# Performance work log

Hardware: AMD Instinct MI355X
Metric: run time of the kernel (lower is better)

The kernel has to match this reference:

```python
import jax, jax.numpy as jnp
import numpy as np

B, T, C = 2, 2048, 2048
NH, NKV, D = 16, 4, 128
N_REP = NH // NKV
THETA = 10000.0


def setup_inputs() -> dict:
    key = jax.random.key(0)
    ks = jax.random.split(key, 5)
    s = 0.02
    return {
        "x": jax.random.normal(ks[0], (B, T, C), dtype=jnp.float32),
        "Wq": jax.random.normal(ks[1], (C, C), dtype=jnp.float32) * s,
        "Wk": jax.random.normal(ks[2], (NKV * D, C), dtype=jnp.float32) * s,
        "Wv": jax.random.normal(ks[3], (NKV * D, C), dtype=jnp.float32) * s,
        "Wo": jax.random.normal(ks[4], (C, C), dtype=jnp.float32) * s,
    }


def _rope(t):
    # t: (B, H, T, D); rotate pairs (even, odd) by angle pos * theta_i
    inv_freq = 1.0 / (THETA ** (jnp.arange(0, D, 2, dtype=jnp.float32) / D))  # (D/2,)
    ang = jnp.arange(T, dtype=jnp.float32)[:, None] * inv_freq[None, :]       # (T, D/2)
    cos, sin = jnp.cos(ang), jnp.sin(ang)
    te, to = t[..., 0::2], t[..., 1::2]
    re = te * cos - to * sin
    ro = te * sin + to * cos
    return jnp.stack([re, ro], axis=-1).reshape(t.shape).astype(t.dtype)


def reference(x, Wq, Wk, Wv, Wo):
    # Projections (Linear: y = x @ W.T)
    q = (x @ Wq.T).reshape(B, T, NH, D).transpose(0, 2, 1, 3)    # (B,NH,T,D)
    k = (x @ Wk.T).reshape(B, T, NKV, D).transpose(0, 2, 1, 3)   # (B,NKV,T,D)
    v = (x @ Wv.T).reshape(B, T, NKV, D).transpose(0, 2, 1, 3)
    q = _rope(q)
    k = _rope(k)
    # GQA: group query heads per kv head instead of materializing repeated K/V
    qg = q.reshape(B, NKV, N_REP, T, D)                          # (B,G,R,T,D)
    scale = 1.0 / jnp.sqrt(jnp.float32(D))
    scores = jnp.einsum("bgrtd,bgsd->bgrts", qg, k) * scale      # (B,G,R,T,T)
    causal = jnp.tril(jnp.ones((T, T), dtype=bool))
    scores = jnp.where(causal, scores, jnp.finfo(scores.dtype).min)
    attn = jax.nn.softmax(scores, axis=-1)
    out = jnp.einsum("bgrts,bgsd->bgrtd", attn, v)               # (B,G,R,T,D)
    out = out.reshape(B, NH, T, D).transpose(0, 2, 1, 3).reshape(B, T, C)
    return out @ Wo.T
```

## Files before the change

### kernel.cpp

```cpp
#include <hip/hip_runtime.h>
#include <hip/hip_bf16.h>
#include <stdint.h>

#define B_   2
#define T_   2048
#define C_   2048
#define NH_  16
#define NKV_ 4
#define D_   128
#define NREP_ 4

typedef __attribute__((ext_vector_type(8))) short bf16x8;
typedef __attribute__((ext_vector_type(4))) float f32x4;

__device__ inline short f2bs(float f) {
    __hip_bfloat16 h = __float2bfloat16(f);
    return *reinterpret_cast<short*>(&h);
}

__device__ inline void gl_lds16(const __hip_bfloat16* g, __hip_bfloat16* l) {
    __builtin_amdgcn_global_load_lds(
        (const __attribute__((address_space(1))) unsigned int*)g,
        (__attribute__((address_space(3))) unsigned int*)l,
        16, 0, 0);
}

__global__ void prep_kernel(const float* __restrict__ x,  const float* __restrict__ Wq,
                            const float* __restrict__ Wk, const float* __restrict__ Wv,
                            const float* __restrict__ Wo,
                            __hip_bfloat16* __restrict__ xb, __hip_bfloat16* __restrict__ wcat,
                            __hip_bfloat16* __restrict__ wob, float2* __restrict__ ropeTab) {
    int tid = blockIdx.x * blockDim.x + threadIdx.x;
    const int CVT_THREADS = 4718592;
    if (tid < CVT_THREADS) {
        int i4 = tid * 4;
        const float* src;
        __hip_bfloat16* dst;
        int off;
        if (i4 < 8388608)       { src = x;  dst = xb;             off = i4; }
        else if (i4 < 12582912) { src = Wq; dst = wcat;           off = i4 - 8388608; }
        else if (i4 < 13631488) { src = Wk; dst = wcat + 4194304; off = i4 - 12582912; }
        else if (i4 < 14680064) { src = Wv; dst = wcat + 5242880; off = i4 - 13631488; }
        else                    { src = Wo; dst = wob;            off = i4 - 14680064; }
        float4 v = *reinterpret_cast<const float4*>(src + off);
        short4 o;
        o.x = f2bs(v.x); o.y = f2bs(v.y); o.z = f2bs(v.z); o.w = f2bs(v.w);
        *reinterpret_cast<short4*>(dst + off) = o;
    } else {
        int e = tid - CVT_THREADS;
        if (e < 131072) {
            int t = e >> 6, p = e & 63;
            float inv = __expf(-(float)p * (9.210340371976184f / 64.0f));
            float ang = (float)t * inv;
            ropeTab[e] = make_float2(cosf(ang), sinf(ang));
        }
    }
}

template <int MODE, int NTN>
__global__ __launch_bounds__(512, 2) void gemm256(
    const __hip_bfloat16* __restrict__ A,
    const __hip_bfloat16* __restrict__ Bm,
    const float2* __restrict__ ropeTab,
    __hip_bfloat16* __restrict__ qo,
    __hip_bfloat16* __restrict__ ko,
    __hip_bfloat16* __restrict__ vT,
    float* __restrict__ Cout) {
    constexpr int K = 2048;
    constexpr int NT = K / 64;
    extern __shared__ char lds[];

    const int tid = threadIdx.x;
    const int lane = tid & 63;
    const int wid = tid >> 6;
    const int wm = wid >> 2, wn = wid & 3;
    const int q16 = lane >> 4, r16 = lane & 15;

    const int cpx = (int)gridDim.x >> 3;
    const int bs = ((int)blockIdx.x & 7) * cpx + ((int)blockIdx.x >> 3);
    const int tm = bs / NTN, tn = bs % NTN;
    const int rmA = tm * 256, rmB = tn * 256;

    char* const aBuf0 = lds + wm * 16384;
    char* const aBuf1 = lds + 32768 + wm * 16384;
    char* const bBuf0 = lds + 65536 + (wn >> 1) * 16384;
    char* const bBuf1 = lds + 65536 + 32768 + (wn >> 1) * 16384;

    const int sw  = (r16 & 7) << 4;
    const int cS0 = (q16 << 4) ^ sw;
    const int cS1 = (64 | (q16 << 4)) ^ sw;
    const int rA128 = r16 * 128;
    const int rB128 = ((wn & 1) * 64 + r16) * 128;

    f32x4 acc[8][4] = {};
    bf16x8 aF[4][2], bF[2][2][2];

#define STG(Mp, rowbase, kstep, ldsoff)                                              \
    { _Pragma("unroll") for (int li = 0; li < 2; li++) {                             \
        const int L_ = li * 8192 + tid * 16;                                         \
        const int rw_ = L_ >> 7;                                                     \
        const int cb_ = (L_ & 127) ^ ((rw_ & 7) << 4);                               \
        gl_lds16(Mp + (size_t)((rowbase) + rw_) * K + (kstep) * 64 + (cb_ >> 1),     \
                 (__hip_bfloat16*)(lds + (ldsoff) + L_));                            \
    } }
#define RDA(base, a)                                                                 \
    { _Pragma("unroll") for (int mi = 0; mi < 4; mi++) {                             \
        const char* p_ = (base) + (a) * 8192 + mi * 2048 + rA128;                    \
        aF[mi][0] = *(const bf16x8*)(p_ + cS0);                                      \
        aF[mi][1] = *(const bf16x8*)(p_ + cS1);                                      \
    } }
#define RDB(base, b)                                                                 \
    { _Pragma("unroll") for (int nj = 0; nj < 2; nj++) {                             \
        const char* p_ = (base) + (b) * 4096 + nj * 2048 + rB128;                    \
        bF[b][nj][0] = *(const bf16x8*)(p_ + cS0);                                   \
        bF[b][nj][1] = *(const bf16x8*)(p_ + cS1);                                   \
    } }
#define MM(a, b)                                                                     \
    { _Pragma("unroll") for (int mi = 0; mi < 4; mi++)                               \
      _Pragma("unroll") for (int nj = 0; nj < 2; nj++) {                             \
        acc[(a)*4+mi][(b)*2+nj] = __builtin_amdgcn_mfma_f32_16x16x32_bf16(           \
            aF[mi][0], bF[(b)][nj][0], acc[(a)*4+mi][(b)*2+nj], 0, 0, 0);            \
        acc[(a)*4+mi][(b)*2+nj] = __builtin_amdgcn_mfma_f32_16x16x32_bf16(           \
            aF[mi][1], bF[(b)][nj][1], acc[(a)*4+mi][(b)*2+nj], 0, 0, 0);            \
    } }
#define BAR  __builtin_amdgcn_s_barrier()
#define LGK0 asm volatile("s_waitcnt lgkmcnt(0)" ::: "memory")
#define VM6  asm volatile("s_waitcnt vmcnt(6)" ::: "memory")
#define VM0  asm volatile("s_waitcnt vmcnt(0)" ::: "memory")
#define PRIO_MM(a, b)                                                                \
    __builtin_amdgcn_s_setprio(1); MM(a, b); __builtin_amdgcn_s_setprio(0)
#define STEP(AB_, BB_, S0_, S2_, S3a_, S3b_, VMW_)                                   \
    RDA(AB_, 0); RDB(BB_, 0); S0_;                                                   \
    BAR; LGK0; PRIO_MM(0, 0); BAR;                                                   \
    RDB(BB_, 1);                                                                     \
    BAR; LGK0; PRIO_MM(0, 1); BAR;                                                   \
    RDA(AB_, 1); S2_;                                                                \
    BAR; LGK0; PRIO_MM(1, 0); BAR;                                                   \
    S3a_; S3b_;                                                                      \
    BAR; LGK0; PRIO_MM(1, 1); VMW_; BAR;

    STG(A,  rmA,       0, 0);
    STG(A,  rmA + 128, 0, 16384);
    STG(Bm, rmB,       0, 65536);
    STG(Bm, rmB + 128, 0, 65536 + 16384);
    STG(A,  rmA,       1, 32768);
    STG(Bm, rmB,       1, 65536 + 32768);
    STG(Bm, rmB + 128, 1, 65536 + 32768 + 16384);
    VM6; BAR;

    for (int u = 0; u < NT - 2; u += 2) {
        STEP(aBuf0, bBuf0,
             STG(A,  rmA + 128, u + 1, 32768 + 16384),
             STG(Bm, rmB,       u + 2, 65536),
             STG(A,  rmA,       u + 2, 0),
             STG(Bm, rmB + 128, u + 2, 65536 + 16384),
             VM6)
        STEP(aBuf1, bBuf1,
             STG(A,  rmA + 128, u + 2, 16384),
             STG(Bm, rmB,       u + 3, 65536 + 32768),
             STG(A,  rmA,       u + 3, 32768),
             STG(Bm, rmB + 128, u + 3, 65536 + 32768 + 16384),
             VM6)
    }
    STEP(aBuf0, bBuf0,
         STG(A, rmA + 128, NT - 1, 32768 + 16384),
         ((void)0), ((void)0), ((void)0),
         VM0)
    STEP(aBuf1, bBuf1, ((void)0), ((void)0), ((void)0), ((void)0), ((void)0))

#undef STEP
#undef PRIO_MM
#undef VM0
#undef VM6
#undef LGK0
#undef BAR
#undef MM
#undef RDB
#undef RDA
#undef STG

    if constexpr (MODE == 0) {
        constexpr int N = NTN * 256;
        float* const cbase = Cout + (size_t)(rmA + wm * 128) * N + tn * 256 + wn * 64 + r16;
#pragma unroll
        for (int Ai = 0; Ai < 8; Ai++)
#pragma unroll
            for (int r = 0; r < 4; r++) {
                float* dst = cbase + (size_t)(Ai * 16 + q16 * 4 + r) * N;
#pragma unroll
                for (int Bi = 0; Bi < 4; Bi++)
                    dst[Bi * 16] = acc[Ai][Bi][r];
            }
    } else {
        const int hb = tn * 2 + (wn >> 1);
        const float sgn = (r16 & 1) ? 1.0f : -1.0f;
#pragma unroll
        for (int Ai = 0; Ai < 8; Ai++)
#pragma unroll
            for (int r = 0; r < 4; r++) {
                const int m = rmA + wm * 128 + Ai * 16 + q16 * 4 + r;
                const int bb = m >> 11, t = m & 2047;
                if (hb < 20) {
                    const float2* tabRow = ropeTab + t * 64;
                    __hip_bfloat16* dst = (hb < 16)
                        ? qo + ((size_t)(bb * NH_ + hb) * T_ + t) * D_
                        : ko + ((size_t)(bb * NKV_ + (hb - 16)) * T_ + t) * D_;
#pragma unroll
                    for (int Bi = 0; Bi < 4; Bi++) {
                        const int dloc = (wn & 1) * 64 + Bi * 16 + r16;
                        float v = acc[Ai][Bi][r];
                        float prt = __shfl_xor(v, 1);
                        float2 cs = tabRow[dloc >> 1];
                        dst[dloc] = __float2bfloat16(fmaf(prt * sgn, cs.y, v * cs.x));
                    }
                } else {
                    __hip_bfloat16* dst = vT + (size_t)(bb * NKV_ + (hb - 20)) * D_ * T_ + t;
#pragma unroll
                    for (int Bi = 0; Bi < 4; Bi++) {
                        const int dloc = (wn & 1) * 64 + Bi * 16 + r16;
                        dst[(size_t)dloc * T_] = __float2bfloat16(acc[Ai][Bi][r]);
                    }
                }
            }
    }
}

__global__ __launch_bounds__(256, 3) void attn_kernel(const __hip_bfloat16* __restrict__ Q,
                                                      const __hip_bfloat16* __restrict__ Kt,
                                                      const __hip_bfloat16* __restrict__ Vt,
                                                      __hip_bfloat16* __restrict__ Ao,
                                                      float* __restrict__ O0,
                                                      float* __restrict__ O1,
                                                      float* __restrict__ l0p,
                                                      float* __restrict__ l1p) {
    __shared__ __hip_bfloat16 Ks[2][4096];
    __shared__ __hip_bfloat16 Vs[2][4096];
    __shared__ __hip_bfloat16 Pl[4][1280];

    const int lane = threadIdx.x & 63, wv = threadIdx.x >> 6;
    const int bg = blockIdx.y;
    const int u  = (int)blockIdx.x;
    int tb, nIt, sIdx;
    if (u < 32)      { tb = u;      nIt = tb + 1;      sIdx = -1; }
    else if (u < 64) { tb = u;      nIt = 32;          sIdx = 0;  }
    else             { tb = u - 32; nIt = tb + 1 - 32; sIdx = 1;  }
    const int sBase = (sIdx == 1) ? 1024 : 0;
    const int b = bg >> 2, g = bg & 3;
    const int h = g * 4 + wv;
    const int t0 = tb * 32;
    const int q16 = lane >> 4, r16 = lane & 15;

    const __hip_bfloat16* qh = Q + ((size_t)((b * NH_ + h) * T_) + t0) * D_;
    const __hip_bfloat16* kh = Kt + (size_t)(b * NKV_ + g) * T_ * D_;
    const __hip_bfloat16* vh = Vt + (size_t)(b * NKV_ + g) * D_ * T_;

    bf16x8 bqA[4], bqB[4];
#pragma unroll
    for (int kk = 0; kk < 4; kk++) {
        bqA[kk] = *reinterpret_cast<const bf16x8*>(qh + (size_t)r16 * D_ + kk * 32 + q16 * 8);
        bqB[kk] = *reinterpret_cast<const bf16x8*>(qh + (size_t)(16 + r16) * D_ + kk * 32 + q16 * 8);
    }

    float liA = 0.f, liB = 0.f;
    f32x4 oA[8], oB[8];
#pragma unroll
    for (int d = 0; d < 8; d++) {
        oA[d] = (f32x4){0.f, 0.f, 0.f, 0.f};
        oB[d] = (f32x4){0.f, 0.f, 0.f, 0.f};
    }

    const float SCL2 = 0.088388347648318447f * 1.4426950408889634f;
    const int tqA = t0 + r16;
    const int tqB = t0 + 16 + r16;

    const __hip_bfloat16* gK = kh + (size_t)((wv & 1) * 16 + r16) * D_ + q16 * 8;
    const __hip_bfloat16* gV = vh + (size_t)(((wv - 2) * 4) * 16 + r16) * T_ + q16 * 8;

#define STAGE(bufi, s0_)                                                        \
    do {                                                                        \
        if (wv < 2) {                                                           \
            const __hip_bfloat16* gp = gK + (size_t)(s0_) * D_;                 \
            __hip_bfloat16* lp = &Ks[bufi][(wv * 4) * 512] + lane * 8;          \
            gl_lds16(gp,      lp);                                              \
            gl_lds16(gp + 32, lp + 512);                                        \
            gl_lds16(gp + 64, lp + 1024);                                      \
            gl_lds16(gp + 96, lp + 1536);                                      \
        } else {                                                                \
            const __hip_bfloat16* gp = gV + (s0_);                              \
            __hip_bfloat16* lp = &Vs[bufi][((wv - 2) * 4) * 512] + lane * 8;    \
            gl_lds16(gp,                      lp);                              \
            gl_lds16(gp + (size_t)16 * T_,    lp + 512);                        \
            gl_lds16(gp + (size_t)32 * T_,    lp + 1024);                      \
            gl_lds16(gp + (size_t)48 * T_,    lp + 1536);                      \
        }                                                                       \
    } while (0)

    STAGE(0, sBase);

    for (int j = 0; j < nIt; j++) {
        const int s0 = sBase + j * 32;
        const int cur = j & 1;
        __syncthreads();
        if (j + 1 < nIt) STAGE(cur ^ 1, s0 + 32);

        f32x4 sc0A = (f32x4){0.f, 0.f, 0.f, 0.f};
        f32x4 sc1A = (f32x4){0.f, 0.f, 0.f, 0.f};
        f32x4 sc0B = (f32x4){0.f, 0.f, 0.f, 0.f};
        f32x4 sc1B = (f32x4){0.f, 0.f, 0.f, 0.f};
        {
            bf16x8 ak[4];
#pragma unroll
            for (int kk = 0; kk < 4; kk++)
                ak[kk] = *reinterpret_cast<const bf16x8*>(&Ks[cur][kk * 512] + lane * 8);
#pragma unroll
            for (int kk = 0; kk < 4; kk++) {
                sc0A = __builtin_amdgcn_mfma_f32_16x16x32_bf16(ak[kk], bqA[kk], sc0A, 0, 0, 0);
                sc0B = __builtin_amdgcn_mfma_f32_16x16x32_bf16(ak[kk], bqB[kk], sc0B, 0, 0, 0);
            }
#pragma unroll
            for (int kk = 0; kk < 4; kk++)
                ak[kk] = *reinterpret_cast<const bf16x8*>(&Ks[cur][(4 + kk) * 512] + lane * 8);
#pragma unroll
            for (int kk = 0; kk < 4; kk++) {
                sc1A = __builtin_amdgcn_mfma_f32_16x16x32_bf16(ak[kk], bqA[kk], sc1A, 0, 0, 0);
                sc1B = __builtin_amdgcn_mfma_f32_16x16x32_bf16(ak[kk], bqB[kk], sc1B, 0, 0, 0);
            }
        }

        ushort4 w0A, w1A, w0B, w1B;
        float psA = 0.f, psB = 0.f;
        if (s0 + 32 > t0) {
#pragma unroll
            for (int r = 0; r < 4; r++) {
                int s_a = s0 + q16 * 4 + r;
                float pa0 = (s_a <= tqA)      ? __builtin_amdgcn_exp2f(sc0A[r] * SCL2) : 0.f;
                float pa1 = (s_a + 16 <= tqA) ? __builtin_amdgcn_exp2f(sc1A[r] * SCL2) : 0.f;
                float pb0 = (s_a <= tqB)      ? __builtin_amdgcn_exp2f(sc0B[r] * SCL2) : 0.f;
                float pb1 = (s_a + 16 <= tqB) ? __builtin_amdgcn_exp2f(sc1B[r] * SCL2) : 0.f;
                psA += pa0 + pa1;
                psB += pb0 + pb1;
                ((unsigned short*)&w0A)[r] = (unsigned short)f2bs(pa0);
                ((unsigned short*)&w1A)[r] = (unsigned short)f2bs(pa1);
                ((unsigned short*)&w0B)[r] = (unsigned short)f2bs(pb0);
                ((unsigned short*)&w1B)[r] = (unsigned short)f2bs(pb1);
            }
        } else {
#pragma unroll
            for (int r = 0; r < 4; r++) {
                float pa0 = __builtin_amdgcn_exp2f(sc0A[r] * SCL2);
                float pa1 = __builtin_amdgcn_exp2f(sc1A[r] * SCL2);
                float pb0 = __builtin_amdgcn_exp2f(sc0B[r] * SCL2);
                float pb1 = __builtin_amdgcn_exp2f(sc1B[r] * SCL2);
                psA += pa0 + pa1;
                psB += pb0 + pb1;
                ((unsigned short*)&w0A)[r] = (unsigned short)f2bs(pa0);
                ((unsigned short*)&w1A)[r] = (unsigned short)f2bs(pa1);
                ((unsigned short*)&w0B)[r] = (unsigned short)f2bs(pb0);
                ((unsigned short*)&w1B)[r] = (unsigned short)f2bs(pb1);
            }
        }
        liA += psA;
        liB += psB;

        *reinterpret_cast<ushort4*>(&Pl[wv][r16 * 40 + q16 * 4]) = w0A;
        *reinterpret_cast<ushort4*>(&Pl[wv][r16 * 40 + 16 + q16 * 4]) = w1A;
        *reinterpret_cast<ushort4*>(&Pl[wv][640 + r16 * 40 + q16 * 4]) = w0B;
        *reinterpret_cast<ushort4*>(&Pl[wv][640 + r16 * 40 + 16 + q16 * 4]) = w1B;
        asm volatile("s_waitcnt lgkmcnt(0)" ::: "memory");
        bf16x8 pfA = *reinterpret_cast<const bf16x8*>(&Pl[wv][r16 * 40 + q16 * 8]);
        bf16x8 pfB = *reinterpret_cast<const bf16x8*>(&Pl[wv][640 + r16 * 40 + q16 * 8]);

#pragma unroll
        for (int d = 0; d < 8; d++) {
            bf16x8 bv = *reinterpret_cast<const bf16x8*>(&Vs[cur][d * 512] + lane * 8);
            oA[d] = __builtin_amdgcn_mfma_f32_16x16x32_bf16(pfA, bv, oA[d], 0, 0, 0);
            oB[d] = __builtin_amdgcn_mfma_f32_16x16x32_bf16(pfB, bv, oB[d], 0, 0, 0);
        }
    }

    liA += __shfl_xor(liA, 16);
    liA += __shfl_xor(liA, 32);
    liB += __shfl_xor(liB, 16);
    liB += __shfl_xor(liB, 32);

    if (sIdx < 0) {
#pragma unroll
        for (int r = 0; r < 4; r++) {
            float lrA = __shfl(liA, q16 * 4 + r, 16);
            float lrB = __shfl(liB, q16 * 4 + r, 16);
            float invA = 1.0f / lrA;
            float invB = 1.0f / lrB;
            int tA = t0 + q16 * 4 + r;
            __hip_bfloat16* dstA = Ao + (size_t)(b * T_ + tA) * C_ + h * D_ + r16;
            __hip_bfloat16* dstB = dstA + (size_t)16 * C_;
#pragma unroll
            for (int d = 0; d < 8; d++) {
                dstA[d * 16] = __float2bfloat16(oA[d][r] * invA);
                dstB[d * 16] = __float2bfloat16(oB[d][r] * invB);
            }
        }
    } else {
        float* Os = (sIdx == 0) ? O0 : O1;
        float* ls = (sIdx == 0) ? l0p : l1p;
        const size_t rb = (size_t)(b * NH_ + h) * 1024 + (size_t)(t0 - 1024);
        if (q16 == 0) {
            ls[rb + r16]      = liA;
            ls[rb + 16 + r16] = liB;
        }
#pragma unroll
        for (int r = 0; r < 4; r++) {
            int rowl = q16 * 4 + r;
            float* dA = Os + (rb + rowl) * 128 + r16;
            float* dB = Os + (rb + 16 + rowl) * 128 + r16;
#pragma unroll
            for (int d = 0; d < 8; d++) {
                dA[d * 16] = oA[d][r];
                dB[d * 16] = oB[d][r];
            }
        }
    }
#undef STAGE
}

__global__ void attn_combine(const float* __restrict__ O0, const float* __restrict__ O1,
                             const float* __restrict__ l0, const float* __restrict__ l1,
                             __hip_bfloat16* __restrict__ Ao) {
    int idx = blockIdx.x * blockDim.x + threadIdx.x;
    int row = idx >> 5, d4 = (idx & 31) << 2;
    int bh = row >> 10, tl = row & 1023;
    int b = bh >> 4, h = bh & 15;
    float inv = 1.0f / (l0[row] + l1[row]);
    float4 a = *reinterpret_cast<const float4*>(O0 + (size_t)row * 128 + d4);
    float4 c = *reinterpret_cast<const float4*>(O1 + (size_t)row * 128 + d4);
    short4 o;
    o.x = f2bs((a.x + c.x) * inv);
    o.y = f2bs((a.y + c.y) * inv);
    o.z = f2bs((a.z + c.z) * inv);
    o.w = f2bs((a.w + c.w) * inv);
    *reinterpret_cast<short4*>(Ao + (size_t)(b * T_ + 1024 + tl) * C_ + h * D_ + d4) = o;
}

extern "C" void kernel_launch(void* const* d_in, const int* in_sizes, int n_in,
                              void* d_out, int out_size, void* d_ws, size_t ws_size,
                              hipStream_t stream) {
    const float* x  = (const float*)d_in[0];
    const float* Wq = (const float*)d_in[1];
    const float* Wk = (const float*)d_in[2];
    const float* Wv = (const float*)d_in[3];
    const float* Wo = (const float*)d_in[4];
    float* out = (float*)d_out;
    char* ws = (char*)d_ws;

    __hip_bfloat16* xb   = (__hip_bfloat16*)(ws + 0);
    __hip_bfloat16* wcat = (__hip_bfloat16*)(ws + 16777216);
    float2*         ropeTab = (float2*)(ws + 29360128);
    __hip_bfloat16* wob  = (__hip_bfloat16*)(ws + 30408704);
    __hip_bfloat16* qatt = (__hip_bfloat16*)(ws + 38797312);
    __hip_bfloat16* katt = (__hip_bfloat16*)(ws + 55574528);
    __hip_bfloat16* vT   = (__hip_bfloat16*)(ws + 59768832);
    __hip_bfloat16* aout = (__hip_bfloat16*)(ws + 63963136);
    float* O0 = (float*)(ws + 0);
    float* O1 = (float*)(ws + 80740352);
    float* l0 = (float*)(ws + 97517568);
    float* l1 = (float*)(ws + 97648640);

    static bool s_attr_done = false;
    if (!s_attr_done) {
        hipFuncSetAttribute(reinterpret_cast<const void*>(&gemm256<1, 12>),
                            hipFuncAttributeMaxDynamicSharedMemorySize, 131072);
        hipFuncSetAttribute(reinterpret_cast<const void*>(&gemm256<0, 8>),
                            hipFuncAttributeMaxDynamicSharedMemorySize, 131072);
        s_attr_done = true;
    }

    const int thr = 256;
    prep_kernel<<<18944, thr, 0, stream>>>(x, Wq, Wk, Wv, Wo, xb, wcat, wob, ropeTab);

    gemm256<1, 12><<<192, 512, 131072, stream>>>(xb, wcat, ropeTab, qatt, katt, vT, nullptr);

    attn_kernel<<<dim3(96, 8), 256, 0, stream>>>(qatt, katt, vT, aout, O0, O1, l0, l1);
    attn_combine<<<(2 * NH_ * 1024 * 32) / thr, thr, 0, stream>>>(O0, O1, l0, l1, aout);

    gemm256<0, 8><<<128, 512, 131072, stream>>>(aout, wob, nullptr, nullptr, nullptr, nullptr, out);
}
```

Measured before the change: 306.5 us.

## Rewrite GEMM pipeline with 32-wide k-slices and parametric N tile

Replaces the hand-scheduled four-phase GEMM mainloop with a simpler double-buffered loop that splits each 64-wide k-step into two 32-column slices, with a 4-row XOR swizzle, and issues the next step's loads before each MFMA batch. The kernel is templated on the N tile width so the output projection uses 256x128 tiles over 256 blocks with less LDS, instead of 128 blocks of 256x256. The aim is to fill more CUs for the small output GEMM and to simplify the overlap of loads and compute. In exchange it loses the fine-grained setprio and barrier interleaving, and the larger number of tiles increases operand reloads.

```diff
diff --git a/kernel.cpp b/kernel.cpp
--- a/kernel.cpp
+++ b/kernel.cpp
@@ -57,8 +57,8 @@
     }
 }
 
-template <int MODE, int NTN>
-__global__ __launch_bounds__(512, 2) void gemm256(
+template <int MODE, int BN, int NTN>
+__global__ __launch_bounds__(512, 2) void gemm_ff(
     const __hip_bfloat16* __restrict__ A,
     const __hip_bfloat16* __restrict__ Bm,
     const float2* __restrict__ ropeTab,
@@ -68,137 +68,117 @@
     float* __restrict__ Cout) {
     constexpr int K = 2048;
     constexpr int NT = K / 64;
+    constexpr int WN = BN / 64;
+    constexpr int WM = 8 / WN;
+    constexpr int RPW = 256 / WM;
+    constexpr int MI_T = RPW / 16;
+    constexpr int BSZ = BN * 64;
+    constexpr int BLOADS = BSZ / 8192;
     extern __shared__ char lds[];
 
     const int tid = threadIdx.x;
     const int lane = tid & 63;
     const int wid = tid >> 6;
-    const int wm = wid >> 2, wn = wid & 3;
+    const int wm = wid / WN, wn = wid % WN;
     const int q16 = lane >> 4, r16 = lane & 15;
 
     const int cpx = (int)gridDim.x >> 3;
     const int bs = ((int)blockIdx.x & 7) * cpx + ((int)blockIdx.x >> 3);
     const int tm = bs / NTN, tn = bs % NTN;
-    const int rmA = tm * 256, rmB = tn * 256;
-
-    char* const aBuf0 = lds + wm * 16384;
-    char* const aBuf1 = lds + 32768 + wm * 16384;
-    char* const bBuf0 = lds + 65536 + (wn >> 1) * 16384;
-    char* const bBuf1 = lds + 65536 + 32768 + (wn >> 1) * 16384;
-
-    const int sw  = (r16 & 7) << 4;
-    const int cS0 = (q16 << 4) ^ sw;
-    const int cS1 = (64 | (q16 << 4)) ^ sw;
-    const int rA128 = r16 * 128;
-    const int rB128 = ((wn & 1) * 64 + r16) * 128;
-
-    f32x4 acc[8][4] = {};
-    bf16x8 aF[4][2], bF[2][2][2];
-
-#define STG(Mp, rowbase, kstep, ldsoff)                                              \
+    const int rmA = tm * 256, rmB = tn * BN;
+
+    const int csw = (q16 << 4) ^ ((r16 & 3) << 4);
+
+    f32x4 acc[MI_T][4] = {};
+    bf16x8 aF[MI_T], bF[4];
+
+#define STG_A(buf_, sl_, kstep_)                                                     \
     { _Pragma("unroll") for (int li = 0; li < 2; li++) {                             \
         const int L_ = li * 8192 + tid * 16;                                         \
-        const int rw_ = L_ >> 7;                                                     \
-        const int cb_ = (L_ & 127) ^ ((rw_ & 7) << 4);                               \
-        gl_lds16(Mp + (size_t)((rowbase) + rw_) * K + (kstep) * 64 + (cb_ >> 1),     \
-                 (__hip_bfloat16*)(lds + (ldsoff) + L_));                            \
+        const int rw_ = L_ >> 6;                                                     \
+        const int cb_ = (L_ & 63) ^ ((rw_ & 3) << 4);                                \
+        gl_lds16(A + (size_t)(rmA + rw_) * K + (kstep_) * 64 + (sl_) * 32 + (cb_ >> 1), \
+                 (__hip_bfloat16*)(lds + (buf_) * 32768 + (sl_) * 16384 + L_));      \
     } }
-#define RDA(base, a)                                                                 \
-    { _Pragma("unroll") for (int mi = 0; mi < 4; mi++) {                             \
-        const char* p_ = (base) + (a) * 8192 + mi * 2048 + rA128;                    \
-        aF[mi][0] = *(const bf16x8*)(p_ + cS0);                                      \
-        aF[mi][1] = *(const bf16x8*)(p_ + cS1);                                      \
+#define STG_B(buf_, sl_, kstep_)                                                     \
+    { _Pragma("unroll") for (int li = 0; li < BLOADS; li++) {                        \
+        const int L_ = li * 8192 + tid * 16;                                         \
+        const int rw_ = L_ >> 6;                                                     \
+        const int cb_ = (L_ & 63) ^ ((rw_ & 3) << 4);                                \
+        gl_lds16(Bm + (size_t)(rmB + rw_) * K + (kstep_) * 64 + (sl_) * 32 + (cb_ >> 1), \
+                 (__hip_bfloat16*)(lds + 65536 + (buf_) * 2 * BSZ + (sl_) * BSZ + L_)); \
     } }
-#define RDB(base, b)                                                                 \
-    { _Pragma("unroll") for (int nj = 0; nj < 2; nj++) {                             \
-        const char* p_ = (base) + (b) * 4096 + nj * 2048 + rB128;                    \
-        bF[b][nj][0] = *(const bf16x8*)(p_ + cS0);                                   \
-        bF[b][nj][1] = *(const bf16x8*)(p_ + cS1);                                   \
-    } }
-#define MM(a, b)                                                                     \
-    { _Pragma("unroll") for (int mi = 0; mi < 4; mi++)                               \
-      _Pragma("unroll") for (int nj = 0; nj < 2; nj++) {                             \
-        acc[(a)*4+mi][(b)*2+nj] = __builtin_amdgcn_mfma_f32_16x16x32_bf16(           \
-            aF[mi][0], bF[(b)][nj][0], acc[(a)*4+mi][(b)*2+nj], 0, 0, 0);            \
-        acc[(a)*4+mi][(b)*2+nj] = __builtin_amdgcn_mfma_f32_16x16x32_bf16(           \
-            aF[mi][1], bF[(b)][nj][1], acc[(a)*4+mi][(b)*2+nj], 0, 0, 0);            \
-    } }
-#define BAR  __builtin_amdgcn_s_barrier()
-#define LGK0 asm volatile("s_waitcnt lgkmcnt(0)" ::: "memory")
-#define VM6  asm volatile("s_waitcnt vmcnt(6)" ::: "memory")
-#define VM0  asm volatile("s_waitcnt vmcnt(0)" ::: "memory")
-#define PRIO_MM(a, b)                                                                \
-    __builtin_amdgcn_s_setprio(1); MM(a, b); __builtin_amdgcn_s_setprio(0)
-#define STEP(AB_, BB_, S0_, S2_, S3a_, S3b_, VMW_)                                   \
-    RDA(AB_, 0); RDB(BB_, 0); S0_;                                                   \
-    BAR; LGK0; PRIO_MM(0, 0); BAR;                                                   \
-    RDB(BB_, 1);                                                                     \
-    BAR; LGK0; PRIO_MM(0, 1); BAR;                                                   \
-    RDA(AB_, 1); S2_;                                                                \
-    BAR; LGK0; PRIO_MM(1, 0); BAR;                                                   \
-    S3a_; S3b_;                                                                      \
-    BAR; LGK0; PRIO_MM(1, 1); VMW_; BAR;
-
-    STG(A,  rmA,       0, 0);
-    STG(A,  rmA + 128, 0, 16384);
-    STG(Bm, rmB,       0, 65536);
-    STG(Bm, rmB + 128, 0, 65536 + 16384);
-    STG(A,  rmA,       1, 32768);
-    STG(Bm, rmB,       1, 65536 + 32768);
-    STG(Bm, rmB + 128, 1, 65536 + 32768 + 16384);
-    VM6; BAR;
-
-    for (int u = 0; u < NT - 2; u += 2) {
-        STEP(aBuf0, bBuf0,
-             STG(A,  rmA + 128, u + 1, 32768 + 16384),
-             STG(Bm, rmB,       u + 2, 65536),
-             STG(A,  rmA,       u + 2, 0),
-             STG(Bm, rmB + 128, u + 2, 65536 + 16384),
-             VM6)
-        STEP(aBuf1, bBuf1,
-             STG(A,  rmA + 128, u + 2, 16384),
-             STG(Bm, rmB,       u + 3, 65536 + 32768),
-             STG(A,  rmA,       u + 3, 32768),
-             STG(Bm, rmB + 128, u + 3, 65536 + 32768 + 16384),
-             VM6)
-    }
-    STEP(aBuf0, bBuf0,
-         STG(A, rmA + 128, NT - 1, 32768 + 16384),
-         ((void)0), ((void)0), ((void)0),
-         VM0)
-    STEP(aBuf1, bBuf1, ((void)0), ((void)0), ((void)0), ((void)0), ((void)0))
-
-#undef STEP
-#undef PRIO_MM
-#undef VM0
-#undef VM6
-#undef LGK0
+#define RD_A(buf_, sl_)                                                              \
+    { _Pragma("unroll") for (int mi = 0; mi < MI_T; mi++)                            \
+        aF[mi] = *(const bf16x8*)(lds + (buf_) * 32768 + (sl_) * 16384 +             \
+                                  (wm * RPW + mi * 16 + r16) * 64 + csw); }
+#define RD_B(buf_, sl_)                                                              \
+    { _Pragma("unroll") for (int bi = 0; bi < 4; bi++)                               \
+        bF[bi] = *(const bf16x8*)(lds + 65536 + (buf_) * 2 * BSZ + (sl_) * BSZ +     \
+                                  (wn * 64 + bi * 16 + r16) * 64 + csw); }
+#define MM_                                                                          \
+    { __builtin_amdgcn_s_setprio(1);                                                 \
+      _Pragma("unroll") for (int mi = 0; mi < MI_T; mi++)                            \
+      _Pragma("unroll") for (int bi = 0; bi < 4; bi++)                               \
+          acc[mi][bi] = __builtin_amdgcn_mfma_f32_16x16x32_bf16(                     \
+              aF[mi], bF[bi], acc[mi][bi], 0, 0, 0);                                 \
+      __builtin_amdgcn_s_setprio(0); }
+#define VMC                                                                          \
+    { if constexpr (BLOADS == 2) { asm volatile("s_waitcnt vmcnt(4)" ::: "memory"); } \
+      else                       { asm volatile("s_waitcnt vmcnt(3)" ::: "memory"); } }
+#define BAR __builtin_amdgcn_s_barrier()
+
+    STG_A(0, 0, 0); STG_B(0, 0, 0);
+    STG_A(0, 1, 0); STG_B(0, 1, 0);
+    VMC; BAR;
+
+    for (int u = 0; u < NT - 1; u++) {
+        const int bf_ = u & 1;
+        RD_A(bf_, 0); RD_B(bf_, 0);
+        STG_A(bf_ ^ 1, 0, u + 1); STG_B(bf_ ^ 1, 0, u + 1);
+        MM_;
+        VMC; BAR;
+        RD_A(bf_, 1); RD_B(bf_, 1);
+        STG_A(bf_ ^ 1, 1, u + 1); STG_B(bf_ ^ 1, 1, u + 1);
+        MM_;
+        VMC; BAR;
+    }
+    {
+        const int bf_ = (NT - 1) & 1;
+        RD_A(bf_, 0); RD_B(bf_, 0);
+        MM_;
+        asm volatile("s_waitcnt vmcnt(0)" ::: "memory"); BAR;
+        RD_A(bf_, 1); RD_B(bf_, 1);
+        MM_;
+    }
 #undef BAR
-#undef MM
-#undef RDB
-#undef RDA
-#undef STG
+#undef VMC
+#undef MM_
+#undef RD_B
+#undef RD_A
+#undef STG_B
+#undef STG_A
 
     if constexpr (MODE == 0) {
-        constexpr int N = NTN * 256;
-        float* const cbase = Cout + (size_t)(rmA + wm * 128) * N + tn * 256 + wn * 64 + r16;
-#pragma unroll
-        for (int Ai = 0; Ai < 8; Ai++)
+        constexpr int N = NTN * BN;
+        float* const cbase = Cout + (size_t)(rmA + wm * RPW) * N + tn * BN + wn * 64 + r16;
+#pragma unroll
+        for (int mi = 0; mi < MI_T; mi++)
 #pragma unroll
             for (int r = 0; r < 4; r++) {
-                float* dst = cbase + (size_t)(Ai * 16 + q16 * 4 + r) * N;
-#pragma unroll
-                for (int Bi = 0; Bi < 4; Bi++)
-                    dst[Bi * 16] = acc[Ai][Bi][r];
+                float* dst = cbase + (size_t)(mi * 16 + q16 * 4 + r) * N;
+#pragma unroll
+                for (int bi = 0; bi < 4; bi++)
+                    dst[bi * 16] = acc[mi][bi][r];
             }
     } else {
         const int hb = tn * 2 + (wn >> 1);
         const float sgn = (r16 & 1) ? 1.0f : -1.0f;
 #pragma unroll
-        for (int Ai = 0; Ai < 8; Ai++)
+        for (int mi = 0; mi < MI_T; mi++)
 #pragma unroll
             for (int r = 0; r < 4; r++) {
-                const int m = rmA + wm * 128 + Ai * 16 + q16 * 4 + r;
+                const int m = rmA + wm * RPW + mi * 16 + q16 * 4 + r;
                 const int bb = m >> 11, t = m & 2047;
                 if (hb < 20) {
                     const float2* tabRow = ropeTab + t * 64;
@@ -206,9 +186,9 @@
                         ? qo + ((size_t)(bb * NH_ + hb) * T_ + t) * D_
                         : ko + ((size_t)(bb * NKV_ + (hb - 16)) * T_ + t) * D_;
 #pragma unroll
-                    for (int Bi = 0; Bi < 4; Bi++) {
-                        const int dloc = (wn & 1) * 64 + Bi * 16 + r16;
-                        float v = acc[Ai][Bi][r];
+                    for (int bi = 0; bi < 4; bi++) {
+                        const int dloc = (wn & 1) * 64 + bi * 16 + r16;
+                        float v = acc[mi][bi][r];
                         float prt = __shfl_xor(v, 1);
                         float2 cs = tabRow[dloc >> 1];
                         dst[dloc] = __float2bfloat16(fmaf(prt * sgn, cs.y, v * cs.x));
@@ -216,9 +196,9 @@
                 } else {
                     __hip_bfloat16* dst = vT + (size_t)(bb * NKV_ + (hb - 20)) * D_ * T_ + t;
 #pragma unroll
-                    for (int Bi = 0; Bi < 4; Bi++) {
-                        const int dloc = (wn & 1) * 64 + Bi * 16 + r16;
-                        dst[(size_t)dloc * T_] = __float2bfloat16(acc[Ai][Bi][r]);
+                    for (int bi = 0; bi < 4; bi++) {
+                        const int dloc = (wn & 1) * 64 + bi * 16 + r16;
+                        dst[(size_t)dloc * T_] = __float2bfloat16(acc[mi][bi][r]);
                     }
                 }
             }
@@ -466,20 +446,20 @@
 
     static bool s_attr_done = false;
     if (!s_attr_done) {
-        hipFuncSetAttribute(reinterpret_cast<const void*>(&gemm256<1, 12>),
+        hipFuncSetAttribute(reinterpret_cast<const void*>(&gemm_ff<1, 256, 12>),
                             hipFuncAttributeMaxDynamicSharedMemorySize, 131072);
-        hipFuncSetAttribute(reinterpret_cast<const void*>(&gemm256<0, 8>),
-                            hipFuncAttributeMaxDynamicSharedMemorySize, 131072);
+        hipFuncSetAttribute(reinterpret_cast<const void*>(&gemm_ff<0, 128, 16>),
+                            hipFuncAttributeMaxDynamicSharedMemorySize, 98304);
         s_attr_done = true;
     }
 
     const int thr = 256;
     prep_kernel<<<18944, thr, 0, stream>>>(x, Wq, Wk, Wv, Wo, xb, wcat, wob, ropeTab);
 
-    gemm256<1, 12><<<192, 512, 131072, stream>>>(xb, wcat, ropeTab, qatt, katt, vT, nullptr);
+    gemm_ff<1, 256, 12><<<192, 512, 131072, stream>>>(xb, wcat, ropeTab, qatt, katt, vT, nullptr);
 
     attn_kernel<<<dim3(96, 8), 256, 0, stream>>>(qatt, katt, vT, aout, O0, O1, l0, l1);
     attn_combine<<<(2 * NH_ * 1024 * 32) / thr, thr, 0, stream>>>(O0, O1, l0, l1, aout);
 
-    gemm256<0, 8><<<128, 512, 131072, stream>>>(aout, wob, nullptr, nullptr, nullptr, nullptr, out);
-}
+    gemm_ff<0, 128, 16><<<256, 512, 98304, stream>>>(aout, wob, nullptr, nullptr, nullptr, nullptr, out);
+}
```

Result: faster. 293.0 us (-4.4%).
